# Performance work log

Measured on AMD Instinct MI355X. Metric: run time of the kernel, lower is better.

Reference implementation:

```python
import jax, jax.numpy as jnp
import numpy as np

EPS = 1e-12

def _normalize(v):
    # matches F.normalize(..., eps): v / max(||v||, eps)
    return v / jnp.maximum(jnp.linalg.norm(v), EPS)

def sn_weight(W, u):
    """One power iteration (num_svs=1, num_itrs=1, eval mode: u not updated).
    W: [out, in] (1x1 conv flattened). u: [1, out].
    u, v are no-grad in torch; sv = v @ W.T @ u'.T carries grad w.r.t. W."""
    v = jax.lax.stop_gradient(_normalize(jax.lax.stop_gradient(u) @ W))          # [1, in]
    u2 = jax.lax.stop_gradient(_normalize(v @ W.T))                              # [1, out]
    sv = (v @ W.T @ u2.T)[0, 0]
    return W / sv

def maxpool2x2(x):
    B, C, H, W = x.shape
    return x.reshape(B, C, H // 2, 2, W // 2, 2).max(axis=(3, 5))

def conv1x1(W, x):
    # W: [out_c, in_c], x: [B, in_c, H, W]
    return jnp.einsum('oc,bchw->bohw', W, x)

def setup_inputs() -> dict:
    key = jax.random.key(0)
    ks = jax.random.split(key, 9)
    ch = 128
    B, H, W = 16, 64, 64
    x = jax.random.normal(ks[0], (B, ch, H, W), dtype=jnp.float32)
    # 1x1 conv weights flattened to [out, in], kaiming-ish scale
    def w(k, o, i):
        return jax.random.normal(k, (o, i), dtype=jnp.float32) * (1.0 / np.sqrt(i))
    w_theta = w(ks[1], ch // 8, ch)
    w_phi   = w(ks[2], ch // 8, ch)
    w_g     = w(ks[3], ch // 2, ch)
    w_o     = w(ks[4], ch, ch // 2)
    u_theta = jax.random.normal(ks[5], (1, ch // 8), dtype=jnp.float32)
    u_phi   = jax.random.normal(ks[6], (1, ch // 8), dtype=jnp.float32)
    u_g     = jax.random.normal(ks[7], (1, ch // 2), dtype=jnp.float32)
    u_o     = jax.random.normal(ks[8], (1, ch), dtype=jnp.float32)
    gamma = jnp.float32(0.7)  # param (init 0.0 in torch; nonzero for a meaningful test)
    return dict(x=x, w_theta=w_theta, w_phi=w_phi, w_g=w_g, w_o=w_o,
                u_theta=u_theta, u_phi=u_phi, u_g=u_g, u_o=u_o, gamma=gamma)

def reference(x, w_theta, w_phi, w_g, w_o, u_theta, u_phi, u_g, u_o, gamma):
    B, C, H, W = x.shape
    Wt = sn_weight(w_theta, u_theta)
    Wp = sn_weight(w_phi, u_phi)
    Wg = sn_weight(w_g, u_g)
    Wo = sn_weight(w_o, u_o)
    theta = conv1x1(Wt, x).reshape(B, C // 8, H * W)               # [B, C/8, HW]
    phi = maxpool2x2(conv1x1(Wp, x)).reshape(B, C // 8, H * W // 4)  # [B, C/8, HW/4]
    g = maxpool2x2(conv1x1(Wg, x)).reshape(B, C // 2, H * W // 4)    # [B, C/2, HW/4]
    beta = jax.nn.softmax(jnp.einsum('bcs,bct->bst', theta, phi), axis=-1)  # [B, HW, HW/4]
    o = jnp.einsum('bct,bst->bcs', g, beta).reshape(B, C // 2, H, W)
    return gamma * conv1x1(Wo, o) + x
```

## Files before the change

kernel.cpp:

```cpp
#include <hip/hip_runtime.h>
#include <hip/hip_bf16.h>


#define U_WN  0
#define U_WO  12288
#define U_TH  20480
#define U_PHI 1069056
#define U_G   1331200

typedef __attribute__((ext_vector_type(8))) short bf16x8;
typedef __attribute__((ext_vector_type(4))) short s16x4;
typedef __attribute__((ext_vector_type(4))) float f32x4;
typedef __attribute__((ext_vector_type(16))) float f32x16;

__device__ inline unsigned short f2b(float f) {
    union { float f; unsigned u; } v; v.f = f;
    unsigned r = v.u + 0x7FFFu + ((v.u >> 16) & 1u);
    return (unsigned short)(r >> 16);
}
__device__ inline float b2f(unsigned short u) {
    union { unsigned u; float f; } v; v.u = ((unsigned)u) << 16; return v.f;
}

__device__ inline unsigned cvtpk_bf16(float lo, float hi) {
    unsigned r;
    asm("s_nop 0\n\tv_cvt_pk_bf16_f32 %0, %1, %2" : "=v"(r) : "v"(lo), "v"(hi));
    return r;
}
__device__ inline void pl32swap(unsigned &a, unsigned &b) {
    asm("s_nop 1\n\tv_permlane32_swap_b32 %0, %1\n\ts_nop 1" : "+v"(a), "+v"(b));
}

__global__ __launch_bounds__(256) void sn4(
        const float* __restrict__ w0, const float* __restrict__ w1,
        const float* __restrict__ w2, const float* __restrict__ w3,
        const float* __restrict__ u0, const float* __restrict__ u1,
        const float* __restrict__ u2, const float* __restrict__ u3,
        unsigned short* __restrict__ wsu) {
    int wi = blockIdx.x;
    const float* W; const float* u; unsigned short* dst; int on, in_;
    if      (wi == 0) { W = w0; u = u0; dst = wsu;          on = 16;  in_ = 128; }
    else if (wi == 1) { W = w1; u = u1; dst = wsu + 2048;   on = 16;  in_ = 128; }
    else if (wi == 2) { W = w2; u = u2; dst = wsu + 4096;   on = 64;  in_ = 128; }
    else              { W = w3; u = u3; dst = wsu + 12288;  on = 128; in_ = 64;  }
    __shared__ float Wl[8320];
    __shared__ float ul[128];
    __shared__ float v[128];
    __shared__ float red[256];
    __shared__ float s_inv;
    int tid = threadIdx.x;
    int n = on * in_;
    int stride = in_ + 1;
    int shift = (in_ == 128) ? 7 : 6;
    int mask = in_ - 1;
    for (int i = tid; i < n; i += 256) {
        int o = i >> shift, j = i & mask;
        Wl[o * stride + j] = W[i];
    }
    if (tid < on) ul[tid] = u[tid];
    __syncthreads();
    float vi = 0.f;
    if (tid < in_) {
        for (int o = 0; o < on; ++o) vi += ul[o] * Wl[o * stride + tid];
    }
    red[tid] = (tid < in_) ? vi * vi : 0.f;
    __syncthreads();
    for (int st = 128; st > 0; st >>= 1) {
        if (tid < st) red[tid] += red[tid + st];
        __syncthreads();
    }
    float inv_nv = 1.0f / fmaxf(sqrtf(red[0]), 1e-12f);
    __syncthreads();
    if (tid < in_) v[tid] = vi * inv_nv;
    __syncthreads();
    float ui = 0.f;
    if (tid < on) {
        for (int i = 0; i < in_; ++i) ui += v[i] * Wl[tid * stride + i];
    }
    red[tid] = (tid < on) ? ui * ui : 0.f;
    __syncthreads();
    for (int st = 128; st > 0; st >>= 1) {
        if (tid < st) red[tid] += red[tid + st];
        __syncthreads();
    }
    if (tid == 0) {
        float nsq = red[0];
        float sv = nsq / fmaxf(sqrtf(nsq), 1e-12f);
        s_inv = 1.0f / sv;
    }
    __syncthreads();
    float inv = s_inv;
    for (int e = tid; e < n; e += 256) {
        int o = e >> shift, j = e & mask;
        dst[e] = f2b(Wl[o * stride + j] * inv);
    }
}

__global__ __launch_bounds__(512, 4) void convpool_mfma(
        const float* __restrict__ x, const unsigned short* __restrict__ wn,
        unsigned short* __restrict__ thetaT, unsigned short* __restrict__ phiT,
        unsigned short* __restrict__ gT) {
    __shared__ unsigned short xT[128 * 136];
    __shared__ unsigned short wnl[96 * 136];
    int tid = threadIdx.x;
    int bb = blockIdx.x >> 5, tile = blockIdx.x & 31;
    int px0 = tile << 7;
    for (int i = tid; i < 1536; i += 512) {
        int r = i >> 4, c8 = (i & 15) * 8;
        *(bf16x8*)&wnl[r * 136 + c8] = *(const bf16x8*)&wn[r * 128 + c8];
    }
    const float4* x4 = (const float4*)x;
    {
        int p4 = tid & 31, cg = (tid >> 5) * 4;
        for (int k = 0; k < 2; ++k) {
            int cb = k * 64 + cg;
            float4 v0 = x4[(bb * 128 + cb + 0) * 1024 + tile * 32 + p4];
            float4 v1 = x4[(bb * 128 + cb + 1) * 1024 + tile * 32 + p4];
            float4 v2 = x4[(bb * 128 + cb + 2) * 1024 + tile * 32 + p4];
            float4 v3 = x4[(bb * 128 + cb + 3) * 1024 + tile * 32 + p4];
            float a0[4] = {v0.x, v0.y, v0.z, v0.w};
            float a1[4] = {v1.x, v1.y, v1.z, v1.w};
            float a2[4] = {v2.x, v2.y, v2.z, v2.w};
            float a3[4] = {v3.x, v3.y, v3.z, v3.w};
#pragma unroll
            for (int j = 0; j < 4; ++j) {
                union { unsigned w[2]; s16x4 v; } pk;
                pk.w[0] = cvtpk_bf16(a0[j], a1[j]);
                pk.w[1] = cvtpk_bf16(a2[j], a3[j]);
                *(s16x4*)&xT[(p4 * 4 + j) * 136 + cb] = pk.v;
            }
        }
    }
    __syncthreads();
    int lane = tid & 63, wv = tid >> 6;
    int q = lane >> 4, l = lane & 15;
    int pxw = wv * 16;
    f32x4 acc[6];
    const f32x4 z4 = {0.f, 0.f, 0.f, 0.f};
#pragma unroll
    for (int nt = 0; nt < 6; ++nt) acc[nt] = z4;
#pragma unroll
    for (int kk = 0; kk < 4; ++kk) {
        bf16x8 a0 = *(const bf16x8*)&xT[(pxw + l) * 136 + kk * 32 + q * 8];
#pragma unroll
        for (int nt = 0; nt < 6; ++nt) {
            bf16x8 bw = *(const bf16x8*)&wnl[(nt * 16 + l) * 136 + kk * 32 + q * 8];
            acc[nt] = __builtin_amdgcn_mfma_f32_16x16x32_bf16(a0, bw, acc[nt], 0, 0, 0);
        }
    }
#pragma unroll
    for (int r = 0; r < 4; ++r) {
        int s = px0 + pxw + q * 4 + r;
        thetaT[(bb * 4096 + s) * 16 + l] = f2b(acc[0][r]);
    }
    __syncthreads();
    unsigned short* poolbuf = wnl;
#pragma unroll
    for (int nt = 1; nt < 6; ++nt) {
        int ch = nt * 16 + l - 16;
#pragma unroll
        for (int r = 0; r < 4; ++r) {
            poolbuf[ch * 132 + pxw + q * 4 + r] = f2b(acc[nt][r]);
        }
    }
    __syncthreads();
    for (int i = tid; i < 2560; i += 512) {
        int tcol = i & 31, ch = i >> 5;
        int base = ch * 132 + tcol * 2;
        float m0 = fmaxf(b2f(poolbuf[base]), b2f(poolbuf[base + 1]));
        float m1 = fmaxf(b2f(poolbuf[base + 64]), b2f(poolbuf[base + 65]));
        float m = fmaxf(m0, m1);
        int t = tile * 32 + tcol;
        if (ch < 16) phiT[(bb * 1024 + t) * 16 + ch] = f2b(m);
        else         gT[(bb * 64 + ch - 16) * 1024 + t] = f2b(m);
    }
}

__global__ __launch_bounds__(256, 3) void attn_out(
        const unsigned short* __restrict__ thetaT,
        const unsigned short* __restrict__ phiT,
        const unsigned short* __restrict__ gT,
        const unsigned short* __restrict__ wo,
        const float* __restrict__ x, const float* __restrict__ gam,
        float* __restrict__ out) {
    __shared__ float ldsO[2][2][2048];
    __shared__ float ldsD[2][2][32];
    int tid = threadIdx.x;
    int kblk = blockIdx.x;
    int vblk = (kblk & 7) * 128 + (kblk >> 3);
    int bb = vblk >> 6, st = vblk & 63;
    int s0 = st << 6;
    int lane = tid & 63, wv = tid >> 6;
    int sg = wv & 1, sp = wv >> 1;
    int sl = lane & 31, hi = lane >> 5;
    int srow = bb * 4096 + s0 + sg * 32 + sl;
    const unsigned short* phiB = phiT + bb * 16384;
    const unsigned short* gB   = gT + bb * 65536;
    int tbase = sp << 9;

    bf16x8 bth = *(const bf16x8*)&thetaT[srow * 16 + hi * 8];

    f32x16 z16;
#pragma unroll
    for (int i = 0; i < 16; ++i) z16[i] = 0.f;
    f32x16 acc0 = z16, acc1 = z16;
    float lp4[4] = {0.f, 0.f, 0.f, 0.f};

    bf16x8 ph0 = *(const bf16x8*)&phiB[(tbase + sl) * 16 + hi * 8];
    bf16x8 ph1 = *(const bf16x8*)&phiB[(tbase + 32 + sl) * 16 + hi * 8];

    for (int tc = 0; tc < 8; ++tc) {
        int t0 = tbase + (tc << 6);
        bf16x8 gf0[4], gf1[4];
#pragma unroll
        for (int kt = 0; kt < 2; ++kt) {
            gf0[kt] = *(const bf16x8*)&gB[(sl) * 1024 + t0 + kt * 16 + hi * 8];
            gf1[kt] = *(const bf16x8*)&gB[(32 + sl) * 1024 + t0 + kt * 16 + hi * 8];
        }
        f32x16 sa = __builtin_amdgcn_mfma_f32_32x32x16_bf16(ph0, bth, z16, 0, 0, 0);
        unsigned u0[8], u1[8];
#pragma unroll
        for (int i = 0; i < 8; ++i) {
            float e0 = __expf(sa[2 * i]);
            float e1 = __expf(sa[2 * i + 1]);
            lp4[0] += e0; lp4[1] += e1;
            u0[i] = cvtpk_bf16(e0, e1);
        }
        __builtin_amdgcn_sched_barrier(0);
        f32x16 sb = __builtin_amdgcn_mfma_f32_32x32x16_bf16(ph1, bth, z16, 0, 0, 0);
        pl32swap(u0[0], u0[2]); pl32swap(u0[1], u0[3]);
        pl32swap(u0[4], u0[6]); pl32swap(u0[5], u0[7]);
#pragma unroll
        for (int kt = 2; kt < 4; ++kt) {
            gf0[kt] = *(const bf16x8*)&gB[(sl) * 1024 + t0 + kt * 16 + hi * 8];
            gf1[kt] = *(const bf16x8*)&gB[(32 + sl) * 1024 + t0 + kt * 16 + hi * 8];
        }
        int t0n = tbase + (((tc + 1) & 7) << 6);
        ph0 = *(const bf16x8*)&phiB[(t0n + sl) * 16 + hi * 8];
        ph1 = *(const bf16x8*)&phiB[(t0n + 32 + sl) * 16 + hi * 8];
#pragma unroll
        for (int i = 0; i < 8; ++i) {
            float e2 = __expf(sb[2 * i]);
            float e3 = __expf(sb[2 * i + 1]);
            lp4[2] += e2; lp4[3] += e3;
            u1[i] = cvtpk_bf16(e2, e3);
        }
        pl32swap(u1[0], u1[2]); pl32swap(u1[1], u1[3]);
        pl32swap(u1[4], u1[6]); pl32swap(u1[5], u1[7]);
        __builtin_amdgcn_s_setprio(1);
        {
            union { unsigned w[4]; bf16x8 v; } pf = {{u0[0], u0[1], u0[2], u0[3]}};
            acc0 = __builtin_amdgcn_mfma_f32_32x32x16_bf16(gf0[0], pf.v, acc0, 0, 0, 0);
            acc1 = __builtin_amdgcn_mfma_f32_32x32x16_bf16(gf1[0], pf.v, acc1, 0, 0, 0);
        }
        {
            union { unsigned w[4]; bf16x8 v; } pf = {{u0[4], u0[5], u0[6], u0[7]}};
            acc0 = __builtin_amdgcn_mfma_f32_32x32x16_bf16(gf0[1], pf.v, acc0, 0, 0, 0);
            acc1 = __builtin_amdgcn_mfma_f32_32x32x16_bf16(gf1[1], pf.v, acc1, 0, 0, 0);
        }
        {
            union { unsigned w[4]; bf16x8 v; } pf = {{u1[0], u1[1], u1[2], u1[3]}};
            acc0 = __builtin_amdgcn_mfma_f32_32x32x16_bf16(gf0[2], pf.v, acc0, 0, 0, 0);
            acc1 = __builtin_amdgcn_mfma_f32_32x32x16_bf16(gf1[2], pf.v, acc1, 0, 0, 0);
        }
        {
            union { unsigned w[4]; bf16x8 v; } pf = {{u1[4], u1[5], u1[6], u1[7]}};
            acc0 = __builtin_amdgcn_mfma_f32_32x32x16_bf16(gf0[3], pf.v, acc0, 0, 0, 0);
            acc1 = __builtin_amdgcn_mfma_f32_32x32x16_bf16(gf1[3], pf.v, acc1, 0, 0, 0);
        }
        __builtin_amdgcn_s_setprio(0);
    }
    float tot = (lp4[0] + lp4[1]) + (lp4[2] + lp4[3]);
    tot += __shfl_xor(tot, 32);

#pragma unroll
    for (int i = 0; i < 16; ++i) {
        int c = (i & 3) + 8 * (i >> 2) + 4 * hi;
        ldsO[sg][sp][c * 32 + sl] = acc0[i];
        ldsO[sg][sp][(32 + c) * 32 + sl] = acc1[i];
    }
    if (hi == 0) ldsD[sg][sp][sl] = tot;
    bf16x8 aw[2][4];
#pragma unroll
    for (int mt = 0; mt < 2; ++mt)
#pragma unroll
        for (int ch = 0; ch < 4; ++ch)
            aw[mt][ch] = *(const bf16x8*)&wo[(sp * 64 + mt * 32 + sl) * 64 + ch * 16 + hi * 8];
    __syncthreads();
    int osp = sp ^ 1;
    tot += ldsD[sg][osp][sl];
    float inv = 1.0f / tot;
#pragma unroll
    for (int i = 0; i < 16; ++i) {
        int c = (i & 3) + 8 * (i >> 2) + 4 * hi;
        acc0[i] += ldsO[sg][osp][c * 32 + sl];
        acc1[i] += ldsO[sg][osp][(32 + c) * 32 + sl];
    }
    unsigned o0[8], o1[8];
#pragma unroll
    for (int i = 0; i < 8; ++i) {
        o0[i] = cvtpk_bf16(acc0[2 * i] * inv, acc0[2 * i + 1] * inv);
        o1[i] = cvtpk_bf16(acc1[2 * i] * inv, acc1[2 * i + 1] * inv);
    }
    pl32swap(o0[0], o0[2]); pl32swap(o0[1], o0[3]);
    pl32swap(o0[4], o0[6]); pl32swap(o0[5], o0[7]);
    pl32swap(o1[0], o1[2]); pl32swap(o1[1], o1[3]);
    pl32swap(o1[4], o1[6]); pl32swap(o1[5], o1[7]);
    bf16x8 bfr[4];
    {
        union { unsigned w[4]; bf16x8 v; } t;
        t.w[0] = o0[0]; t.w[1] = o0[1]; t.w[2] = o0[2]; t.w[3] = o0[3]; bfr[0] = t.v;
        t.w[0] = o0[4]; t.w[1] = o0[5]; t.w[2] = o0[6]; t.w[3] = o0[7]; bfr[1] = t.v;
        t.w[0] = o1[0]; t.w[1] = o1[1]; t.w[2] = o1[2]; t.w[3] = o1[3]; bfr[2] = t.v;
        t.w[0] = o1[4]; t.w[1] = o1[5]; t.w[2] = o1[6]; t.w[3] = o1[7]; bfr[3] = t.v;
    }
    f32x16 d0 = z16, d1 = z16;
#pragma unroll
    for (int ch = 0; ch < 4; ++ch) {
        d0 = __builtin_amdgcn_mfma_f32_32x32x16_bf16(aw[0][ch], bfr[ch], d0, 0, 0, 0);
        d1 = __builtin_amdgcn_mfma_f32_32x32x16_bf16(aw[1][ch], bfr[ch], d1, 0, 0, 0);
    }
    float gm = gam[0];
    int scol = s0 + sg * 32 + sl;
#pragma unroll
    for (int i = 0; i < 16; ++i) {
        int r = (i & 3) + 8 * (i >> 2) + 4 * hi;
        int a0 = (bb * 128 + sp * 64 + r) * 4096 + scol;
        int a1 = (bb * 128 + sp * 64 + 32 + r) * 4096 + scol;
        out[a0] = gm * d0[i] + x[a0];
        out[a1] = gm * d1[i] + x[a1];
    }
}

extern "C" void kernel_launch(void* const* d_in, const int* in_sizes, int n_in,
                              void* d_out, int out_size, void* d_ws, size_t ws_size,
                              hipStream_t stream) {
    const float* x  = (const float*)d_in[0];
    const float* wt = (const float*)d_in[1];
    const float* wp = (const float*)d_in[2];
    const float* wg = (const float*)d_in[3];
    const float* wo = (const float*)d_in[4];
    const float* ut = (const float*)d_in[5];
    const float* up = (const float*)d_in[6];
    const float* ug = (const float*)d_in[7];
    const float* uo = (const float*)d_in[8];
    const float* gm = (const float*)d_in[9];
    unsigned short* wsu = (unsigned short*)d_ws;
    float* out = (float*)d_out;

    sn4<<<4, 256, 0, stream>>>(wt, wp, wg, wo, ut, up, ug, uo, wsu);
    convpool_mfma<<<512, 512, 0, stream>>>(x, wsu + U_WN,
                                           wsu + U_TH, wsu + U_PHI, wsu + U_G);
    attn_out<<<1024, 256, 0, stream>>>(wsu + U_TH, wsu + U_PHI, wsu + U_G,
                                       wsu + U_WO, x, gm, out);
}
```

Baseline: 148.1 us.

## Stage g tiles through double-buffered swizzled LDS shared by both wave groups

The attention-output kernel now cooperatively loads each 64-column chunk of g into a double-buffered, XOR-swizzled LDS tile with a barrier per iteration, instead of every wave reading its g fragments directly from global memory. The two s-groups (sg) share the same g tile, so this halves redundant global traffic. The LDS buffer is reused for the final cross-wave reduction. Occupancy hint is raised from 3 to 4 blocks per CU, which may pressure registers; the added per-iteration __syncthreads may cost latency hiding.

```diff
diff --git a/kernel.cpp b/kernel.cpp
--- a/kernel.cpp
+++ b/kernel.cpp
@@ -176,15 +176,16 @@
     }
 }
 
-__global__ __launch_bounds__(256, 3) void attn_out(
+__global__ __launch_bounds__(256, 4) void attn_out(
         const unsigned short* __restrict__ thetaT,
         const unsigned short* __restrict__ phiT,
         const unsigned short* __restrict__ gT,
         const unsigned short* __restrict__ wo,
         const float* __restrict__ x, const float* __restrict__ gam,
         float* __restrict__ out) {
-    __shared__ float ldsO[2][2][2048];
+    __shared__ unsigned short gl[2][2][4096];
     __shared__ float ldsD[2][2][32];
+    float* ldsOf = (float*)&gl[0][0][0];
     int tid = threadIdx.x;
     int kblk = blockIdx.x;
     int vblk = (kblk & 7) * 128 + (kblk >> 3);
@@ -198,7 +199,26 @@
     const unsigned short* gB   = gT + bb * 65536;
     int tbase = sp << 9;
 
+    int sidx = tid & 127, shalf = tid >> 7;
+    int src_c = sidx >> 1, spos = sidx & 1;
+    const unsigned short* gsrc = gB + src_c * 1024 + shalf * 512 + spos * 32;
+    unsigned short* glw = &gl[0][0][0];
+    int wrow = src_c * 64;
+    int wsw  = (src_c & 7) << 3;
+    int wo_0 = (spos * 32 + 0)  ^ wsw, wo_1 = (spos * 32 + 8)  ^ wsw;
+    int wo_2 = (spos * 32 + 16) ^ wsw, wo_3 = (spos * 32 + 24) ^ wsw;
+
     bf16x8 bth = *(const bf16x8*)&thetaT[srow * 16 + hi * 8];
+
+    {
+        bf16x8 r0 = *(const bf16x8*)&gsrc[0];
+        bf16x8 r1 = *(const bf16x8*)&gsrc[8];
+        bf16x8 r2 = *(const bf16x8*)&gsrc[16];
+        bf16x8 r3 = *(const bf16x8*)&gsrc[24];
+        unsigned short* d = &glw[shalf * 4096 + wrow];
+        *(bf16x8*)&d[wo_0] = r0; *(bf16x8*)&d[wo_1] = r1;
+        *(bf16x8*)&d[wo_2] = r2; *(bf16x8*)&d[wo_3] = r3;
+    }
 
     f32x16 z16;
 #pragma unroll
@@ -208,14 +228,18 @@
 
     bf16x8 ph0 = *(const bf16x8*)&phiB[(tbase + sl) * 16 + hi * 8];
     bf16x8 ph1 = *(const bf16x8*)&phiB[(tbase + 32 + sl) * 16 + hi * 8];
-
+    __syncthreads();
+
+    int rsw = (sl & 7) << 3;
     for (int tc = 0; tc < 8; ++tc) {
-        int t0 = tbase + (tc << 6);
-        bf16x8 gf0[4], gf1[4];
-#pragma unroll
-        for (int kt = 0; kt < 2; ++kt) {
-            gf0[kt] = *(const bf16x8*)&gB[(sl) * 1024 + t0 + kt * 16 + hi * 8];
-            gf1[kt] = *(const bf16x8*)&gB[(32 + sl) * 1024 + t0 + kt * 16 + hi * 8];
+        int buf = tc & 1;
+        bf16x8 r0, r1, r2, r3;
+        if (tc < 7) {
+            const unsigned short* gs = gsrc + (tc + 1) * 64;
+            r0 = *(const bf16x8*)&gs[0];
+            r1 = *(const bf16x8*)&gs[8];
+            r2 = *(const bf16x8*)&gs[16];
+            r3 = *(const bf16x8*)&gs[24];
         }
         f32x16 sa = __builtin_amdgcn_mfma_f32_32x32x16_bf16(ph0, bth, z16, 0, 0, 0);
         unsigned u0[8], u1[8];
@@ -230,11 +254,6 @@
         f32x16 sb = __builtin_amdgcn_mfma_f32_32x32x16_bf16(ph1, bth, z16, 0, 0, 0);
         pl32swap(u0[0], u0[2]); pl32swap(u0[1], u0[3]);
         pl32swap(u0[4], u0[6]); pl32swap(u0[5], u0[7]);
-#pragma unroll
-        for (int kt = 2; kt < 4; ++kt) {
-            gf0[kt] = *(const bf16x8*)&gB[(sl) * 1024 + t0 + kt * 16 + hi * 8];
-            gf1[kt] = *(const bf16x8*)&gB[(32 + sl) * 1024 + t0 + kt * 16 + hi * 8];
-        }
         int t0n = tbase + (((tc + 1) & 7) << 6);
         ph0 = *(const bf16x8*)&phiB[(t0n + sl) * 16 + hi * 8];
         ph1 = *(const bf16x8*)&phiB[(t0n + 32 + sl) * 16 + hi * 8];
@@ -247,37 +266,58 @@
         }
         pl32swap(u1[0], u1[2]); pl32swap(u1[1], u1[3]);
         pl32swap(u1[4], u1[6]); pl32swap(u1[5], u1[7]);
+        const unsigned short* glr = &glw[(buf * 2 + sp) * 4096];
         __builtin_amdgcn_s_setprio(1);
         {
+            int co = (0 * 16 + hi * 8) ^ rsw;
+            bf16x8 gf0 = *(const bf16x8*)&glr[sl * 64 + co];
+            bf16x8 gf1 = *(const bf16x8*)&glr[(32 + sl) * 64 + co];
             union { unsigned w[4]; bf16x8 v; } pf = {{u0[0], u0[1], u0[2], u0[3]}};
-            acc0 = __builtin_amdgcn_mfma_f32_32x32x16_bf16(gf0[0], pf.v, acc0, 0, 0, 0);
-            acc1 = __builtin_amdgcn_mfma_f32_32x32x16_bf16(gf1[0], pf.v, acc1, 0, 0, 0);
+            acc0 = __builtin_amdgcn_mfma_f32_32x32x16_bf16(gf0, pf.v, acc0, 0, 0, 0);
+            acc1 = __builtin_amdgcn_mfma_f32_32x32x16_bf16(gf1, pf.v, acc1, 0, 0, 0);
         }
         {
+            int co = (1 * 16 + hi * 8) ^ rsw;
+            bf16x8 gf0 = *(const bf16x8*)&glr[sl * 64 + co];
+            bf16x8 gf1 = *(const bf16x8*)&glr[(32 + sl) * 64 + co];
             union { unsigned w[4]; bf16x8 v; } pf = {{u0[4], u0[5], u0[6], u0[7]}};
-            acc0 = __builtin_amdgcn_mfma_f32_32x32x16_bf16(gf0[1], pf.v, acc0, 0, 0, 0);
-            acc1 = __builtin_amdgcn_mfma_f32_32x32x16_bf16(gf1[1], pf.v, acc1, 0, 0, 0);
+            acc0 = __builtin_amdgcn_mfma_f32_32x32x16_bf16(gf0, pf.v, acc0, 0, 0, 0);
+            acc1 = __builtin_amdgcn_mfma_f32_32x32x16_bf16(gf1, pf.v, acc1, 0, 0, 0);
         }
         {
+            int co = (2 * 16 + hi * 8) ^ rsw;
+            bf16x8 gf0 = *(const bf16x8*)&glr[sl * 64 + co];
+            bf16x8 gf1 = *(const bf16x8*)&glr[(32 + sl) * 64 + co];
             union { unsigned w[4]; bf16x8 v; } pf = {{u1[0], u1[1], u1[2], u1[3]}};
-            acc0 = __builtin_amdgcn_mfma_f32_32x32x16_bf16(gf0[2], pf.v, acc0, 0, 0, 0);
-            acc1 = __builtin_amdgcn_mfma_f32_32x32x16_bf16(gf1[2], pf.v, acc1, 0, 0, 0);
+            acc0 = __builtin_amdgcn_mfma_f32_32x32x16_bf16(gf0, pf.v, acc0, 0, 0, 0);
+            acc1 = __builtin_amdgcn_mfma_f32_32x32x16_bf16(gf1, pf.v, acc1, 0, 0, 0);
         }
         {
+            int co = (3 * 16 + hi * 8) ^ rsw;
+            bf16x8 gf0 = *(const bf16x8*)&glr[sl * 64 + co];
+            bf16x8 gf1 = *(const bf16x8*)&glr[(32 + sl) * 64 + co];
             union { unsigned w[4]; bf16x8 v; } pf = {{u1[4], u1[5], u1[6], u1[7]}};
-            acc0 = __builtin_amdgcn_mfma_f32_32x32x16_bf16(gf0[3], pf.v, acc0, 0, 0, 0);
-            acc1 = __builtin_amdgcn_mfma_f32_32x32x16_bf16(gf1[3], pf.v, acc1, 0, 0, 0);
+            acc0 = __builtin_amdgcn_mfma_f32_32x32x16_bf16(gf0, pf.v, acc0, 0, 0, 0);
+            acc1 = __builtin_amdgcn_mfma_f32_32x32x16_bf16(gf1, pf.v, acc1, 0, 0, 0);
         }
         __builtin_amdgcn_s_setprio(0);
-    }
+        if (tc < 7) {
+            unsigned short* d = &glw[((buf ^ 1) * 2 + shalf) * 4096 + wrow];
+            *(bf16x8*)&d[wo_0] = r0; *(bf16x8*)&d[wo_1] = r1;
+            *(bf16x8*)&d[wo_2] = r2; *(bf16x8*)&d[wo_3] = r3;
+            __syncthreads();
+        }
+    }
+    __syncthreads();
+
     float tot = (lp4[0] + lp4[1]) + (lp4[2] + lp4[3]);
     tot += __shfl_xor(tot, 32);
 
 #pragma unroll
     for (int i = 0; i < 16; ++i) {
         int c = (i & 3) + 8 * (i >> 2) + 4 * hi;
-        ldsO[sg][sp][c * 32 + sl] = acc0[i];
-        ldsO[sg][sp][(32 + c) * 32 + sl] = acc1[i];
+        ldsOf[(sg * 2 + sp) * 2048 + c * 32 + sl] = acc0[i];
+        ldsOf[(sg * 2 + sp) * 2048 + (32 + c) * 32 + sl] = acc1[i];
     }
     if (hi == 0) ldsD[sg][sp][sl] = tot;
     bf16x8 aw[2][4];
@@ -293,8 +333,8 @@
 #pragma unroll
     for (int i = 0; i < 16; ++i) {
         int c = (i & 3) + 8 * (i >> 2) + 4 * hi;
-        acc0[i] += ldsO[sg][osp][c * 32 + sl];
-        acc1[i] += ldsO[sg][osp][(32 + c) * 32 + sl];
+        acc0[i] += ldsOf[(sg * 2 + osp) * 2048 + c * 32 + sl];
+        acc1[i] += ldsOf[(sg * 2 + osp) * 2048 + (32 + c) * 32 + sl];
     }
     unsigned o0[8], o1[8];
 #pragma unroll
```

New measurement: 134.0 us. -9.5%, faster.
